# Kernel optimization log

Hardware: AMD Instinct MI355X
Metric: run time of the kernel (lower is better)

## Reference

```python
import jax, jax.numpy as jnp
import numpy as np
from jax import lax

D = 2048
B = 8
T = 1024

def setup_inputs() -> dict:
    key = jax.random.key(0)
    ks = jax.random.split(key, 6)
    s = 1.0 / np.sqrt(D)
    return {
        "x": jax.random.normal(ks[0], (B, T, D), dtype=jnp.float32),
        "h0": jnp.zeros((B, D), dtype=jnp.float32),
        "W_in": jax.random.normal(ks[1], (D, D), dtype=jnp.float32) * s,
        "W_x": jax.random.normal(ks[2], (D, D), dtype=jnp.float32) * s,
        "W_h": jax.random.normal(ks[3], (D, D), dtype=jnp.float32) * (0.5 * s),
        "b": jnp.zeros((D,), dtype=jnp.float32),
        "log_alpha": jnp.asarray(np.log(0.5), dtype=jnp.float32),
        "W_out": jax.random.normal(ks[4], (D, D), dtype=jnp.float32) * s,
    }


def reference(x, h0, W_in, W_x, W_h, b, log_alpha, W_out):
    # x: [B,T,D] -> in_proj + silu pre-activation
    u = jax.nn.silu(jnp.einsum('btd,ed->bte', x, W_in))  # [B,T,D]
    alpha = jnp.exp(log_alpha)
    # Precompute input contribution for all steps: [T,B,D]
    wx_all = jnp.einsum('btd,ed->tbe', u, W_x) + b

    def step(h_prev, wx_t):
        pre = h_prev @ W_h.T + wx_t                  # [B,D]
        h_new = h_prev + alpha * jnp.tanh(pre)
        out = h_new * jax.nn.silu(h_new)             # self-gating
        return h_new, out

    _, outs = lax.scan(step, h0, wx_all)             # outs: [T,B,D]
    y = jnp.einsum('tbd,ed->bte', outs, W_out)       # out_proj -> [B,T,D]
    return y
```

## Files before the change

### kernel.cpp

```cpp
#include <hip/hip_runtime.h>

#define DEV static __device__ __forceinline__

typedef _Float16 half8  __attribute__((ext_vector_type(8)));
typedef _Float16 half4v __attribute__((ext_vector_type(4)));
typedef float    floatx4 __attribute__((ext_vector_type(4)));
typedef unsigned int u32;
typedef unsigned long long u64;
typedef u32 u32x4 __attribute__((ext_vector_type(4)));

#define SPLIT_S 1024.0f
#define SPLIT_R (1.0f / 1024.0f)

DEV void gl_lds16(const _Float16* g, _Float16* l) {
  __builtin_amdgcn_global_load_lds(
      (const __attribute__((address_space(1))) u32*)g,
      (__attribute__((address_space(3))) u32*)l, 16, 0, 0);
}

DEV u32x4 llc_load16(u64 addr) {
  u32x4 r;
  asm volatile("global_load_dwordx4 %0, %1, off sc0 sc1"
               : "=v"(r) : "v"(addr));
  return r;
}
DEV void llc_store8(u64 addr, u64 v) {
  asm volatile("global_store_dwordx2 %0, %1, off sc0 sc1"
               :: "v"(addr), "v"(v) : "memory");
}
DEV void llc_store4(u64 addr, int v) {
  asm volatile("global_store_dword %0, %1, off sc0 sc1"
               :: "v"(addr), "v"(v) : "memory");
}

DEV float fast_tanh(float x) {
  const float e = __expf(2.0f * fabsf(x));
  return copysignf(1.0f - 2.0f / (1.0f + e), x);
}

__global__ __launch_bounds__(256) void k_convert(
    const float* __restrict__ wout, const float* __restrict__ h0,
    _Float16* __restrict__ WoutF, char* __restrict__ hpub,
    int* __restrict__ flags)
{
  if (blockIdx.x == 0 && threadIdx.x < 128) flags[threadIdx.x] = 0;
  const int NW4 = (2048 * 2048) / 4;
  for (int i = blockIdx.x * 256 + threadIdx.x; i < NW4; i += gridDim.x * 256) {
    const float4 v = ((const float4*)wout)[i];
    half4v o;
    o[0] = (_Float16)v.x; o[1] = (_Float16)v.y;
    o[2] = (_Float16)v.z; o[3] = (_Float16)v.w;
    ((half4v*)WoutF)[i] = o;
  }
  for (int id = blockIdx.x * 256 + threadIdx.x; id < 2048; id += gridDim.x * 256) {
    const int c = id >> 3, b = id & 7;
    union { _Float16 h[8]; u32x4 v; } hi, lo;
#pragma unroll
    for (int j = 0; j < 8; ++j) {
      const float v = h0[b * 2048 + c * 8 + j];
      const _Float16 h = (_Float16)v;
      hi.h[j] = h;
      lo.h[j] = (_Float16)((v - (float)h) * SPLIT_S);
    }
    *(u32x4*)(hpub + c * 128 + b * 16)         = hi.v;
    *(u32x4*)(hpub + 32768 + c * 128 + b * 16) = lo.v;
  }
}

template <int EPI>
__global__ __launch_bounds__(256) void k_gemm_split(
    const float* __restrict__ A, const float* __restrict__ B,
    float* __restrict__ C, const float* __restrict__ bias,
    int M, int N, int K)
{
  __shared__ _Float16 Ah[4096], Al[4096], Bh[4096], Bl[4096];
  const int tid  = threadIdx.x;
  const int lane = tid & 63, wave = tid >> 6;
  const int wm = wave >> 1, wn = wave & 1;
  const int tm = blockIdx.y * 128, tn = blockIdx.x * 128;
  const int lr = lane & 15, lk = lane >> 4;

  floatx4 acch[4][4] = {};
  floatx4 accl[4][4] = {};

  for (int k0 = 0; k0 < K; k0 += 32) {
    float4 av[4], bv[4];
#pragma unroll
    for (int q = 0; q < 4; ++q) {
      const int c = tid + q * 256;
      const int rr = c >> 3, cc = (c & 7) * 4;
      av[q] = *(const float4*)(A + (size_t)(tm + rr) * K + k0 + cc);
      bv[q] = *(const float4*)(B + (size_t)(tn + rr) * K + k0 + cc);
    }
    __syncthreads();
#pragma unroll
    for (int q = 0; q < 4; ++q) {
      const int c = tid + q * 256;
      const int rr = c >> 3, cc = (c & 7) * 4;
      half4v ah, al, bh, bl;
#pragma unroll
      for (int j = 0; j < 4; ++j) {
        const float xa = av[q][j], xb = bv[q][j];
        const _Float16 ha = (_Float16)xa, hb = (_Float16)xb;
        ah[j] = ha; al[j] = (_Float16)((xa - (float)ha) * SPLIT_S);
        bh[j] = hb; bl[j] = (_Float16)((xb - (float)hb) * SPLIT_S);
      }
      *(half4v*)(Ah + rr * 32 + cc) = ah;
      *(half4v*)(Al + rr * 32 + cc) = al;
      *(half4v*)(Bh + rr * 32 + cc) = bh;
      *(half4v*)(Bl + rr * 32 + cc) = bl;
    }
    __syncthreads();

    half8 fah[4], fal[4], fbh[4], fbl[4];
#pragma unroll
    for (int mi = 0; mi < 4; ++mi) {
      const int off = (wm * 64 + mi * 16 + lr) * 32 + lk * 8;
      fah[mi] = *(const half8*)(Ah + off);
      fal[mi] = *(const half8*)(Al + off);
    }
#pragma unroll
    for (int ni = 0; ni < 4; ++ni) {
      const int off = (wn * 64 + ni * 16 + lr) * 32 + lk * 8;
      fbh[ni] = *(const half8*)(Bh + off);
      fbl[ni] = *(const half8*)(Bl + off);
    }
#pragma unroll
    for (int mi = 0; mi < 4; ++mi)
#pragma unroll
      for (int ni = 0; ni < 4; ++ni) {
        acch[mi][ni] = __builtin_amdgcn_mfma_f32_16x16x32_f16(fah[mi], fbh[ni], acch[mi][ni], 0, 0, 0);
        accl[mi][ni] = __builtin_amdgcn_mfma_f32_16x16x32_f16(
            fah[mi], fbl[ni],
            __builtin_amdgcn_mfma_f32_16x16x32_f16(fal[mi], fbh[ni], accl[mi][ni], 0, 0, 0),
            0, 0, 0);
      }
  }

#pragma unroll
  for (int mi = 0; mi < 4; ++mi)
#pragma unroll
    for (int ni = 0; ni < 4; ++ni) {
      const int gcol = tn + wn * 64 + ni * 16 + lr;
#pragma unroll
      for (int r = 0; r < 4; ++r) {
        const int grow = tm + wm * 64 + mi * 16 + lk * 4 + r;
        const float v = acch[mi][ni][r] + accl[mi][ni][r] * SPLIT_R;
        if (EPI == 0) {
          C[(size_t)grow * N + gcol] = v / (1.0f + __expf(-v));
        } else {
          const int tt = grow & 1023, bb = grow >> 10;
          C[(size_t)(tt * 8 + bb) * N + gcol] = v + bias[gcol];
        }
      }
    }
}

__global__ __launch_bounds__(256) void k_gemm_out(
    const _Float16* __restrict__ A, const _Float16* __restrict__ B,
    float* __restrict__ C, int M, int N, int K)
{
  __shared__ _Float16 As[4096];
  __shared__ _Float16 Bs[4096];
  const int tid  = threadIdx.x;
  const int lane = tid & 63, wave = tid >> 6;
  const int wm = wave >> 1, wn = wave & 1;
  const int tm = blockIdx.y * 128, tn = blockIdx.x * 128;
  const int lr = lane & 15, lk = lane >> 4;
  const int r0 = tid >> 2;
  const int c0 = (tid & 3) * 8;

  floatx4 acc[4][4] = {};

  for (int k0 = 0; k0 < K; k0 += 32) {
#pragma unroll
    for (int c = 0; c < 2; ++c) {
      const int row = c * 64 + r0;
      gl_lds16(A + (size_t)(tm + row) * K + k0 + c0, As + c * 2048 + wave * 512);
      gl_lds16(B + (size_t)(tn + row) * K + k0 + c0, Bs + c * 2048 + wave * 512);
    }
    __syncthreads();

    half8 af[4], bf[4];
#pragma unroll
    for (int mi = 0; mi < 4; ++mi)
      af[mi] = *(const half8*)(As + (wm * 64 + mi * 16 + lr) * 32 + lk * 8);
#pragma unroll
    for (int ni = 0; ni < 4; ++ni)
      bf[ni] = *(const half8*)(Bs + (wn * 64 + ni * 16 + lr) * 32 + lk * 8);
#pragma unroll
    for (int mi = 0; mi < 4; ++mi)
#pragma unroll
      for (int ni = 0; ni < 4; ++ni)
        acc[mi][ni] = __builtin_amdgcn_mfma_f32_16x16x32_f16(af[mi], bf[ni], acc[mi][ni], 0, 0, 0);
    __syncthreads();
  }

#pragma unroll
  for (int mi = 0; mi < 4; ++mi)
#pragma unroll
    for (int ni = 0; ni < 4; ++ni) {
      const int gcol = tn + wn * 64 + ni * 16 + lr;
#pragma unroll
      for (int r = 0; r < 4; ++r) {
        const int grow = tm + wm * 64 + mi * 16 + lk * 4 + r;
        C[(size_t)grow * N + gcol] = acc[mi][ni][r] * 8.0f;
      }
    }
}

__global__ __launch_bounds__(256, 1) void k_recur(
    const float* __restrict__ Wh, const float* __restrict__ wxp,
    const float* __restrict__ h0p, const float* __restrict__ lalpha,
    _Float16* __restrict__ outs, char* __restrict__ h_pub, int* flags)
{
  __shared__ float red[256 * 4];
  const int tid = threadIdx.x;
  const int lane = tid & 63, wave = tid >> 6;
  const int g = blockIdx.x;
  const int e0 = g * 16;
  const int lr = lane & 15, lk = lane >> 4;
  const int lrc = lr & 7;
  const float alpha = __expf(lalpha[0]);

  half8 afh[16], afl[16];
#pragma unroll
  for (int ks = 0; ks < 16; ++ks) {
    const float* wp = Wh + (size_t)(e0 + lr) * 2048 + wave * 512 + ks * 32 + lk * 8;
    const float4 f0 = *(const float4*)wp;
    const float4 f1 = *(const float4*)(wp + 4);
    half8 h, l;
#pragma unroll
    for (int j = 0; j < 4; ++j) {
      const float a0 = ((const float*)&f0)[j], a1 = ((const float*)&f1)[j];
      const _Float16 h0_ = (_Float16)a0;
      const _Float16 h1_ = (_Float16)a1;
      h[j]     = h0_; l[j]     = (_Float16)((a0 - (float)h0_) * SPLIT_S);
      h[j + 4] = h1_; l[j + 4] = (_Float16)((a1 - (float)h1_) * SPLIT_S);
    }
    afh[ks] = h; afl[ks] = l;
  }

  const bool owner = (tid < 64) && (lr < 8);
  float hr0 = 0.f, hr1 = 0.f, hr2 = 0.f, hr3 = 0.f;
  if (owner) {
    const float4 hv = *(const float4*)(h0p + (size_t)lr * 2048 + e0 + lk * 4);
    hr0 = hv.x; hr1 = hv.y; hr2 = hv.z; hr3 = hv.w;
  }

  const u64 hbase = (u64)h_pub;
  const u64 flag_base = (u64)flags;
  const u64 gb_off = (u64)((wave * 64 + lk) * 128 + lrc * 16);

  for (int t = 0; t < 1024; ++t) {
    float4 wv = {0.f, 0.f, 0.f, 0.f};
    if (owner) wv = *(const float4*)(wxp + (size_t)(t * 8 + lr) * 2048 + e0 + lk * 4);

    if (t > 0 && wave == 0) {
      const u64* fp = (const u64*)flags + lane;
      for (;;) {
        const u64 fv = __hip_atomic_load(fp, __ATOMIC_RELAXED, __HIP_MEMORY_SCOPE_AGENT);
        if (__all(((int)fv >= t) && ((int)(fv >> 32) >= t))) break;
        __builtin_amdgcn_s_sleep(1);
      }
    }
    __syncthreads();

    const u64 pb = hbase + (u64)(t & 1) * 65536 + gb_off;
    u32x4 sh[16], sl[16];
#pragma unroll
    for (int ks = 0; ks < 16; ++ks) sh[ks] = llc_load16(pb + (u64)ks * 512);
#pragma unroll
    for (int ks = 0; ks < 16; ++ks) sl[ks] = llc_load16(pb + 32768 + (u64)ks * 512);
    asm volatile("s_waitcnt vmcnt(16)" ::: "memory");
    __builtin_amdgcn_sched_barrier(0);

    floatx4 ph[4] = {};
    floatx4 pl[4] = {};
#pragma unroll
    for (int ks = 0; ks < 16; ++ks) {
      const half8 bh = __builtin_bit_cast(half8, sh[ks]);
      ph[ks & 3] = __builtin_amdgcn_mfma_f32_16x16x32_f16(afh[ks], bh, ph[ks & 3], 0, 0, 0);
      pl[ks & 3] = __builtin_amdgcn_mfma_f32_16x16x32_f16(afl[ks], bh, pl[ks & 3], 0, 0, 0);
    }
    asm volatile("s_waitcnt vmcnt(0)" ::: "memory");
    __builtin_amdgcn_sched_barrier(0);

#pragma unroll
    for (int ks = 0; ks < 16; ++ks) {
      const half8 bl = __builtin_bit_cast(half8, sl[ks]);
      pl[ks & 3] = __builtin_amdgcn_mfma_f32_16x16x32_f16(afh[ks], bl, pl[ks & 3], 0, 0, 0);
    }
    const floatx4 pt = (ph[0] + ph[1] + ph[2] + ph[3]) +
                       (pl[0] + pl[1] + pl[2] + pl[3]) * SPLIT_R;
    *(floatx4*)&red[(wave * 64 + lane) * 4] = pt;
    __syncthreads();

    if (tid < 64) {
      const floatx4* R = (const floatx4*)red;
      const floatx4 s = R[lane] + R[64 + lane] + R[128 + lane] + R[192 + lane];
      union { _Float16 h[4]; u64 u; } hv, lv, ov;
      if (owner) {
        hr0 += alpha * fast_tanh(s[0] + wv.x);
        hr1 += alpha * fast_tanh(s[1] + wv.y);
        hr2 += alpha * fast_tanh(s[2] + wv.z);
        hr3 += alpha * fast_tanh(s[3] + wv.w);
        hv.h[0] = (_Float16)hr0; hv.h[1] = (_Float16)hr1;
        hv.h[2] = (_Float16)hr2; hv.h[3] = (_Float16)hr3;
        lv.h[0] = (_Float16)((hr0 - (float)hv.h[0]) * SPLIT_S);
        lv.h[1] = (_Float16)((hr1 - (float)hv.h[1]) * SPLIT_S);
        lv.h[2] = (_Float16)((hr2 - (float)hv.h[2]) * SPLIT_S);
        lv.h[3] = (_Float16)((hr3 - (float)hv.h[3]) * SPLIT_S);
        const u64 dst = hbase + (u64)((t + 1) & 1) * 65536 +
                        (u64)((2 * g + (lk >> 1)) * 128 + lr * 16 + (lk & 1) * 8);
        llc_store8(dst,         hv.u);
        llc_store8(dst + 32768, lv.u);
      }
      asm volatile("s_waitcnt vmcnt(0)" ::: "memory");
      if (lane == 0) llc_store4(flag_base + (u64)g * 4, t + 1);
      if (owner) {
        ov.h[0] = (_Float16)((hr0 * hr0 / (1.f + __expf(-hr0))) * 0.125f);
        ov.h[1] = (_Float16)((hr1 * hr1 / (1.f + __expf(-hr1))) * 0.125f);
        ov.h[2] = (_Float16)((hr2 * hr2 / (1.f + __expf(-hr2))) * 0.125f);
        ov.h[3] = (_Float16)((hr3 * hr3 / (1.f + __expf(-hr3))) * 0.125f);
        *(u64*)(outs + (size_t)(lr * 1024 + t) * 2048 + e0 + lk * 4) = ov.u;
      }
    }
  }
}

extern "C" void kernel_launch(void* const* d_in, const int* in_sizes, int n_in,
                              void* d_out, int out_size, void* d_ws, size_t ws_size,
                              hipStream_t stream)
{
  (void)in_sizes; (void)n_in; (void)out_size; (void)ws_size;
  const float* x    = (const float*)d_in[0];
  const float* h0   = (const float*)d_in[1];
  const float* Win  = (const float*)d_in[2];
  const float* Wx   = (const float*)d_in[3];
  const float* Wh   = (const float*)d_in[4];
  const float* bias = (const float*)d_in[5];
  const float* lal  = (const float*)d_in[6];
  const float* Wout = (const float*)d_in[7];

  char* ws = (char*)d_ws;
  float*    U     = (float*)(ws);
  _Float16* OUTS  = (_Float16*)(ws);
  _Float16* WoutF = (_Float16*)(ws + 67108864);
  char*     hpub  = ws + 75497472;
  int*      flags = (int*)(ws + 75628544);
  float*    wxbuf = (float*)d_out;

  const dim3 gg(16, 64);

  k_convert<<<512, 256, 0, stream>>>(Wout, h0, WoutF, hpub, flags);
  k_gemm_split<0><<<gg, 256, 0, stream>>>(x, Win, U, nullptr, 8192, 2048, 2048);
  k_gemm_split<1><<<gg, 256, 0, stream>>>(U, Wx, wxbuf, bias, 8192, 2048, 2048);
  k_recur<<<128, 256, 0, stream>>>(Wh, wxbuf, h0, lal, OUTS, hpub, flags);
  k_gemm_out<<<gg, 256, 0, stream>>>(OUTS, WoutF, (float*)d_out, 8192, 2048, 2048);
}
```

Measured before the change: 4.513 ms.

## Halve recurrence blocks to 64 with 32 columns each; publish via atomic swaps

The persistent recurrence kernel now runs on 64 blocks, each owning 32 hidden columns, so there are two 16-row MFMA tiles per wave and every lane of wave 0 owns outputs. This halves the number of flags each block polls per step and the number of cross-block participants in the per-step barrier. Hidden-state and flag publication switch from sc0/sc1 stores to global atomic swaps, which are meant to resolve at the shared cache level. The cost is twice the MFMA work and register-held weights per block, with fewer CUs active.

```diff
diff --git a/kernel.cpp b/kernel.cpp
--- a/kernel.cpp
+++ b/kernel.cpp
@@ -24,12 +24,12 @@
                : "=v"(r) : "v"(addr));
   return r;
 }
-DEV void llc_store8(u64 addr, u64 v) {
-  asm volatile("global_store_dwordx2 %0, %1, off sc0 sc1"
+DEV void mall_swap8(u64 addr, u64 v) {
+  asm volatile("global_atomic_swap_x2 %0, %1, off"
                :: "v"(addr), "v"(v) : "memory");
 }
-DEV void llc_store4(u64 addr, int v) {
-  asm volatile("global_store_dword %0, %1, off sc0 sc1"
+DEV void mall_swap4(u64 addr, int v) {
+  asm volatile("global_atomic_swap %0, %1, off"
                :: "v"(addr), "v"(v) : "memory");
 }
 
@@ -43,7 +43,7 @@
     _Float16* __restrict__ WoutF, char* __restrict__ hpub,
     int* __restrict__ flags)
 {
-  if (blockIdx.x == 0 && threadIdx.x < 128) flags[threadIdx.x] = 0;
+  if (blockIdx.x == 0 && threadIdx.x < 64) flags[threadIdx.x] = 0;
   const int NW4 = (2048 * 2048) / 4;
   for (int i = blockIdx.x * 256 + threadIdx.x; i < NW4; i += gridDim.x * 256) {
     const float4 v = ((const float4*)wout)[i];
@@ -214,37 +214,40 @@
     const float* __restrict__ h0p, const float* __restrict__ lalpha,
     _Float16* __restrict__ outs, char* __restrict__ h_pub, int* flags)
 {
-  __shared__ float red[256 * 4];
+  __shared__ float red[8 * 64 * 4];
   const int tid = threadIdx.x;
   const int lane = tid & 63, wave = tid >> 6;
   const int g = blockIdx.x;
-  const int e0 = g * 16;
+  const int e0 = g * 32;
   const int lr = lane & 15, lk = lane >> 4;
   const int lrc = lr & 7;
   const float alpha = __expf(lalpha[0]);
 
-  half8 afh[16], afl[16];
-#pragma unroll
-  for (int ks = 0; ks < 16; ++ks) {
-    const float* wp = Wh + (size_t)(e0 + lr) * 2048 + wave * 512 + ks * 32 + lk * 8;
-    const float4 f0 = *(const float4*)wp;
-    const float4 f1 = *(const float4*)(wp + 4);
-    half8 h, l;
-#pragma unroll
-    for (int j = 0; j < 4; ++j) {
-      const float a0 = ((const float*)&f0)[j], a1 = ((const float*)&f1)[j];
-      const _Float16 h0_ = (_Float16)a0;
-      const _Float16 h1_ = (_Float16)a1;
-      h[j]     = h0_; l[j]     = (_Float16)((a0 - (float)h0_) * SPLIT_S);
-      h[j + 4] = h1_; l[j + 4] = (_Float16)((a1 - (float)h1_) * SPLIT_S);
-    }
-    afh[ks] = h; afl[ks] = l;
-  }
-
-  const bool owner = (tid < 64) && (lr < 8);
+  half8 afh[2][16], afl[2][16];
+#pragma unroll
+  for (int m = 0; m < 2; ++m)
+#pragma unroll
+    for (int ks = 0; ks < 16; ++ks) {
+      const float* wp = Wh + (size_t)(e0 + m * 16 + lr) * 2048 + wave * 512 + ks * 32 + lk * 8;
+      const float4 f0 = *(const float4*)wp;
+      const float4 f1 = *(const float4*)(wp + 4);
+      half8 h, l;
+#pragma unroll
+      for (int j = 0; j < 4; ++j) {
+        const float a0 = ((const float*)&f0)[j], a1 = ((const float*)&f1)[j];
+        const _Float16 h0_ = (_Float16)a0;
+        const _Float16 h1_ = (_Float16)a1;
+        h[j]     = h0_; l[j]     = (_Float16)((a0 - (float)h0_) * SPLIT_S);
+        h[j + 4] = h1_; l[j + 4] = (_Float16)((a1 - (float)h1_) * SPLIT_S);
+      }
+      afh[m][ks] = h; afl[m][ks] = l;
+    }
+
+  const int ob = lane & 7, ocg = lane >> 3;
+  const bool owner = (tid < 64);
   float hr0 = 0.f, hr1 = 0.f, hr2 = 0.f, hr3 = 0.f;
   if (owner) {
-    const float4 hv = *(const float4*)(h0p + (size_t)lr * 2048 + e0 + lk * 4);
+    const float4 hv = *(const float4*)(h0p + (size_t)ob * 2048 + e0 + ocg * 4);
     hr0 = hv.x; hr1 = hv.y; hr2 = hv.z; hr3 = hv.w;
   }
 
@@ -254,13 +257,14 @@
 
   for (int t = 0; t < 1024; ++t) {
     float4 wv = {0.f, 0.f, 0.f, 0.f};
-    if (owner) wv = *(const float4*)(wxp + (size_t)(t * 8 + lr) * 2048 + e0 + lk * 4);
+    if (owner) wv = *(const float4*)(wxp + (size_t)(t * 8 + ob) * 2048 + e0 + ocg * 4);
 
     if (t > 0 && wave == 0) {
-      const u64* fp = (const u64*)flags + lane;
+      const u64* fp = (const u64*)flags + (lane & 31);
       for (;;) {
         const u64 fv = __hip_atomic_load(fp, __ATOMIC_RELAXED, __HIP_MEMORY_SCOPE_AGENT);
-        if (__all(((int)fv >= t) && ((int)(fv >> 32) >= t))) break;
+        const bool ok = (lane < 32) ? (((int)fv >= t) && ((int)(fv >> 32) >= t)) : true;
+        if (__all(ok)) break;
         __builtin_amdgcn_s_sleep(1);
       }
     }
@@ -275,13 +279,15 @@
     asm volatile("s_waitcnt vmcnt(16)" ::: "memory");
     __builtin_amdgcn_sched_barrier(0);
 
-    floatx4 ph[4] = {};
-    floatx4 pl[4] = {};
+    floatx4 ph[2][2] = {};
+    floatx4 pl[2][2] = {};
 #pragma unroll
     for (int ks = 0; ks < 16; ++ks) {
       const half8 bh = __builtin_bit_cast(half8, sh[ks]);
-      ph[ks & 3] = __builtin_amdgcn_mfma_f32_16x16x32_f16(afh[ks], bh, ph[ks & 3], 0, 0, 0);
-      pl[ks & 3] = __builtin_amdgcn_mfma_f32_16x16x32_f16(afl[ks], bh, pl[ks & 3], 0, 0, 0);
+      ph[0][ks & 1] = __builtin_amdgcn_mfma_f32_16x16x32_f16(afh[0][ks], bh, ph[0][ks & 1], 0, 0, 0);
+      pl[0][ks & 1] = __builtin_amdgcn_mfma_f32_16x16x32_f16(afl[0][ks], bh, pl[0][ks & 1], 0, 0, 0);
+      ph[1][ks & 1] = __builtin_amdgcn_mfma_f32_16x16x32_f16(afh[1][ks], bh, ph[1][ks & 1], 0, 0, 0);
+      pl[1][ks & 1] = __builtin_amdgcn_mfma_f32_16x16x32_f16(afl[1][ks], bh, pl[1][ks & 1], 0, 0, 0);
     }
     asm volatile("s_waitcnt vmcnt(0)" ::: "memory");
     __builtin_amdgcn_sched_barrier(0);
@@ -289,42 +295,45 @@
 #pragma unroll
     for (int ks = 0; ks < 16; ++ks) {
       const half8 bl = __builtin_bit_cast(half8, sl[ks]);
-      pl[ks & 3] = __builtin_amdgcn_mfma_f32_16x16x32_f16(afh[ks], bl, pl[ks & 3], 0, 0, 0);
-    }
-    const floatx4 pt = (ph[0] + ph[1] + ph[2] + ph[3]) +
-                       (pl[0] + pl[1] + pl[2] + pl[3]) * SPLIT_R;
-    *(floatx4*)&red[(wave * 64 + lane) * 4] = pt;
-    __syncthreads();
-
-    if (tid < 64) {
+      pl[0][ks & 1] = __builtin_amdgcn_mfma_f32_16x16x32_f16(afh[0][ks], bl, pl[0][ks & 1], 0, 0, 0);
+      pl[1][ks & 1] = __builtin_amdgcn_mfma_f32_16x16x32_f16(afh[1][ks], bl, pl[1][ks & 1], 0, 0, 0);
+    }
+#pragma unroll
+    for (int m = 0; m < 2; ++m) {
+      const floatx4 pt = (ph[m][0] + ph[m][1]) + (pl[m][0] + pl[m][1]) * SPLIT_R;
+      *(floatx4*)&red[((wave * 2 + m) * 64 + lane) * 4] = pt;
+    }
+    __syncthreads();
+
+    if (owner) {
       const floatx4* R = (const floatx4*)red;
-      const floatx4 s = R[lane] + R[64 + lane] + R[128 + lane] + R[192 + lane];
+      const int fi = (ocg & 3) * 16 + ob;
+      const int mm = ocg >> 2;
+      const floatx4 s = R[(0 * 2 + mm) * 64 + fi] + R[(1 * 2 + mm) * 64 + fi] +
+                        R[(2 * 2 + mm) * 64 + fi] + R[(3 * 2 + mm) * 64 + fi];
       union { _Float16 h[4]; u64 u; } hv, lv, ov;
-      if (owner) {
-        hr0 += alpha * fast_tanh(s[0] + wv.x);
-        hr1 += alpha * fast_tanh(s[1] + wv.y);
-        hr2 += alpha * fast_tanh(s[2] + wv.z);
-        hr3 += alpha * fast_tanh(s[3] + wv.w);
-        hv.h[0] = (_Float16)hr0; hv.h[1] = (_Float16)hr1;
-        hv.h[2] = (_Float16)hr2; hv.h[3] = (_Float16)hr3;
-        lv.h[0] = (_Float16)((hr0 - (float)hv.h[0]) * SPLIT_S);
-        lv.h[1] = (_Float16)((hr1 - (float)hv.h[1]) * SPLIT_S);
-        lv.h[2] = (_Float16)((hr2 - (float)hv.h[2]) * SPLIT_S);
-        lv.h[3] = (_Float16)((hr3 - (float)hv.h[3]) * SPLIT_S);
-        const u64 dst = hbase + (u64)((t + 1) & 1) * 65536 +
-                        (u64)((2 * g + (lk >> 1)) * 128 + lr * 16 + (lk & 1) * 8);
-        llc_store8(dst,         hv.u);
-        llc_store8(dst + 32768, lv.u);
-      }
+      hr0 += alpha * fast_tanh(s[0] + wv.x);
+      hr1 += alpha * fast_tanh(s[1] + wv.y);
+      hr2 += alpha * fast_tanh(s[2] + wv.z);
+      hr3 += alpha * fast_tanh(s[3] + wv.w);
+      hv.h[0] = (_Float16)hr0; hv.h[1] = (_Float16)hr1;
+      hv.h[2] = (_Float16)hr2; hv.h[3] = (_Float16)hr3;
+      lv.h[0] = (_Float16)((hr0 - (float)hv.h[0]) * SPLIT_S);
+      lv.h[1] = (_Float16)((hr1 - (float)hv.h[1]) * SPLIT_S);
+      lv.h[2] = (_Float16)((hr2 - (float)hv.h[2]) * SPLIT_S);
+      lv.h[3] = (_Float16)((hr3 - (float)hv.h[3]) * SPLIT_S);
+      const u64 dst = hbase + (u64)((t + 1) & 1) * 65536 +
+                      (u64)((4 * g + (ocg >> 1)) * 128 + ob * 16 + (ocg & 1) * 8);
+      mall_swap8(dst,         hv.u);
+      mall_swap8(dst + 32768, lv.u);
       asm volatile("s_waitcnt vmcnt(0)" ::: "memory");
-      if (lane == 0) llc_store4(flag_base + (u64)g * 4, t + 1);
-      if (owner) {
-        ov.h[0] = (_Float16)((hr0 * hr0 / (1.f + __expf(-hr0))) * 0.125f);
-        ov.h[1] = (_Float16)((hr1 * hr1 / (1.f + __expf(-hr1))) * 0.125f);
-        ov.h[2] = (_Float16)((hr2 * hr2 / (1.f + __expf(-hr2))) * 0.125f);
-        ov.h[3] = (_Float16)((hr3 * hr3 / (1.f + __expf(-hr3))) * 0.125f);
-        *(u64*)(outs + (size_t)(lr * 1024 + t) * 2048 + e0 + lk * 4) = ov.u;
-      }
+      if (lane == 0) mall_swap4(flag_base + (u64)g * 4, t + 1);
+      ov.h[0] = (_Float16)((hr0 * hr0 / (1.f + __expf(-hr0))) * 0.125f);
+      ov.h[1] = (_Float16)((hr1 * hr1 / (1.f + __expf(-hr1))) * 0.125f);
+      ov.h[2] = (_Float16)((hr2 * hr2 / (1.f + __expf(-hr2))) * 0.125f);
+      ov.h[3] = (_Float16)((hr3 * hr3 / (1.f + __expf(-hr3))) * 0.125f);
+      *(u64*)(outs + (size_t)(ob * 1024 + t) * 2048 + e0 + ocg * 4) = ov.u;
+    } else if (tid == 64) {
     }
   }
 }
@@ -356,6 +365,6 @@
   k_convert<<<512, 256, 0, stream>>>(Wout, h0, WoutF, hpub, flags);
   k_gemm_split<0><<<gg, 256, 0, stream>>>(x, Win, U, nullptr, 8192, 2048, 2048);
   k_gemm_split<1><<<gg, 256, 0, stream>>>(U, Wx, wxbuf, bias, 8192, 2048, 2048);
-  k_recur<<<128, 256, 0, stream>>>(Wh, wxbuf, h0, lal, OUTS, hpub, flags);
+  k_recur<<<64, 256, 0, stream>>>(Wh, wxbuf, h0, lal, OUTS, hpub, flags);
   k_gemm_out<<<gg, 256, 0, stream>>>(OUTS, WoutF, (float*)d_out, 8192, 2048, 2048);
 }
```

New measurement: 4.653 ms. +3.1%, slower.

## Pre-split U and W_x into fp16 hi/lo pairs for second GEMM

Applied to the files above, without the earlier changes.

The first GEMM epilogue now writes the SiLU output as fp16 hi/lo halves instead of fp32, and W_x is pre-split into hi/lo fp16 by the convert kernel. The second GEMM then streams these halves directly into LDS with global_load_lds, skipping the per-tile fp32-to-split conversion in registers. W_out conversion moves to a separate kernel after gemm2 so it can reuse U's workspace region. This trades an extra kernel launch and an extra W_x conversion pass for lighter loads and less ALU work in the second GEMM.

```diff
diff --git a/kernel.cpp b/kernel.cpp
--- a/kernel.cpp
+++ b/kernel.cpp
@@ -39,11 +39,43 @@
 }
 
 __global__ __launch_bounds__(256) void k_convert(
-    const float* __restrict__ wout, const float* __restrict__ h0,
-    _Float16* __restrict__ WoutF, char* __restrict__ hpub,
-    int* __restrict__ flags)
+    const float* __restrict__ wx, const float* __restrict__ h0,
+    _Float16* __restrict__ Wxhi, _Float16* __restrict__ Wxlo,
+    char* __restrict__ hpub, int* __restrict__ flags)
 {
   if (blockIdx.x == 0 && threadIdx.x < 128) flags[threadIdx.x] = 0;
+  const int NW4 = (2048 * 2048) / 4;
+  for (int i = blockIdx.x * 256 + threadIdx.x; i < NW4; i += gridDim.x * 256) {
+    const float4 v = ((const float4*)wx)[i];
+    half4v h, l;
+#pragma unroll
+    for (int j = 0; j < 4; ++j) {
+      const float a = ((const float*)&v)[j];
+      const _Float16 hh = (_Float16)a;
+      h[j] = hh;
+      l[j] = (_Float16)((a - (float)hh) * SPLIT_S);
+    }
+    ((half4v*)Wxhi)[i] = h;
+    ((half4v*)Wxlo)[i] = l;
+  }
+  for (int id = blockIdx.x * 256 + threadIdx.x; id < 2048; id += gridDim.x * 256) {
+    const int c = id >> 3, b = id & 7;
+    union { _Float16 h[8]; u32x4 v; } hi, lo;
+#pragma unroll
+    for (int j = 0; j < 8; ++j) {
+      const float v = h0[b * 2048 + c * 8 + j];
+      const _Float16 h = (_Float16)v;
+      hi.h[j] = h;
+      lo.h[j] = (_Float16)((v - (float)h) * SPLIT_S);
+    }
+    *(u32x4*)(hpub + c * 128 + b * 16)         = hi.v;
+    *(u32x4*)(hpub + 32768 + c * 128 + b * 16) = lo.v;
+  }
+}
+
+__global__ __launch_bounds__(256) void k_convert2(
+    const float* __restrict__ wout, _Float16* __restrict__ WoutF)
+{
   const int NW4 = (2048 * 2048) / 4;
   for (int i = blockIdx.x * 256 + threadIdx.x; i < NW4; i += gridDim.x * 256) {
     const float4 v = ((const float4*)wout)[i];
@@ -52,25 +84,11 @@
     o[2] = (_Float16)v.z; o[3] = (_Float16)v.w;
     ((half4v*)WoutF)[i] = o;
   }
-  for (int id = blockIdx.x * 256 + threadIdx.x; id < 2048; id += gridDim.x * 256) {
-    const int c = id >> 3, b = id & 7;
-    union { _Float16 h[8]; u32x4 v; } hi, lo;
-#pragma unroll
-    for (int j = 0; j < 8; ++j) {
-      const float v = h0[b * 2048 + c * 8 + j];
-      const _Float16 h = (_Float16)v;
-      hi.h[j] = h;
-      lo.h[j] = (_Float16)((v - (float)h) * SPLIT_S);
-    }
-    *(u32x4*)(hpub + c * 128 + b * 16)         = hi.v;
-    *(u32x4*)(hpub + 32768 + c * 128 + b * 16) = lo.v;
-  }
-}
-
-template <int EPI>
-__global__ __launch_bounds__(256) void k_gemm_split(
+}
+
+__global__ __launch_bounds__(256) void k_gemm1(
     const float* __restrict__ A, const float* __restrict__ B,
-    float* __restrict__ C, const float* __restrict__ bias,
+    _Float16* __restrict__ Chi, _Float16* __restrict__ Clo,
     int M, int N, int K)
 {
   __shared__ _Float16 Ah[4096], Al[4096], Bh[4096], Bl[4096];
@@ -146,12 +164,82 @@
       for (int r = 0; r < 4; ++r) {
         const int grow = tm + wm * 64 + mi * 16 + lk * 4 + r;
         const float v = acch[mi][ni][r] + accl[mi][ni][r] * SPLIT_R;
-        if (EPI == 0) {
-          C[(size_t)grow * N + gcol] = v / (1.0f + __expf(-v));
-        } else {
-          const int tt = grow & 1023, bb = grow >> 10;
-          C[(size_t)(tt * 8 + bb) * N + gcol] = v + bias[gcol];
-        }
+        const float s = v / (1.0f + __expf(-v));
+        const _Float16 sh = (_Float16)s;
+        Chi[(size_t)grow * N + gcol] = sh;
+        Clo[(size_t)grow * N + gcol] = (_Float16)((s - (float)sh) * SPLIT_S);
+      }
+    }
+}
+
+__global__ __launch_bounds__(256) void k_gemm2(
+    const _Float16* __restrict__ Ahi, const _Float16* __restrict__ Alo,
+    const _Float16* __restrict__ Bhi, const _Float16* __restrict__ Blo,
+    float* __restrict__ C, const float* __restrict__ bias,
+    int M, int N, int K)
+{
+  __shared__ _Float16 Ah[4096], Al[4096], Bh[4096], Bl[4096];
+  const int tid  = threadIdx.x;
+  const int lane = tid & 63, wave = tid >> 6;
+  const int wm = wave >> 1, wn = wave & 1;
+  const int tm = blockIdx.y * 128, tn = blockIdx.x * 128;
+  const int lr = lane & 15, lk = lane >> 4;
+  const int r0 = tid >> 2;
+  const int c0 = (tid & 3) * 8;
+
+  floatx4 acch[4][4] = {};
+  floatx4 accl[4][4] = {};
+
+  for (int k0 = 0; k0 < K; k0 += 32) {
+#pragma unroll
+    for (int c = 0; c < 2; ++c) {
+      const int row = c * 64 + r0;
+      const size_t aoff = (size_t)(tm + row) * K + k0 + c0;
+      const size_t boff = (size_t)(tn + row) * K + k0 + c0;
+      gl_lds16(Ahi + aoff, Ah + c * 2048 + wave * 512);
+      gl_lds16(Alo + aoff, Al + c * 2048 + wave * 512);
+      gl_lds16(Bhi + boff, Bh + c * 2048 + wave * 512);
+      gl_lds16(Blo + boff, Bl + c * 2048 + wave * 512);
+    }
+    __syncthreads();
+
+    half8 fah[4], fal[4], fbh[4], fbl[4];
+#pragma unroll
+    for (int mi = 0; mi < 4; ++mi) {
+      const int off = (wm * 64 + mi * 16 + lr) * 32 + lk * 8;
+      fah[mi] = *(const half8*)(Ah + off);
+      fal[mi] = *(const half8*)(Al + off);
+    }
+#pragma unroll
+    for (int ni = 0; ni < 4; ++ni) {
+      const int off = (wn * 64 + ni * 16 + lr) * 32 + lk * 8;
+      fbh[ni] = *(const half8*)(Bh + off);
+      fbl[ni] = *(const half8*)(Bl + off);
+    }
+#pragma unroll
+    for (int mi = 0; mi < 4; ++mi)
+#pragma unroll
+      for (int ni = 0; ni < 4; ++ni) {
+        acch[mi][ni] = __builtin_amdgcn_mfma_f32_16x16x32_f16(fah[mi], fbh[ni], acch[mi][ni], 0, 0, 0);
+        accl[mi][ni] = __builtin_amdgcn_mfma_f32_16x16x32_f16(
+            fah[mi], fbl[ni],
+            __builtin_amdgcn_mfma_f32_16x16x32_f16(fal[mi], fbh[ni], accl[mi][ni], 0, 0, 0),
+            0, 0, 0);
+      }
+    __syncthreads();
+  }
+
+#pragma unroll
+  for (int mi = 0; mi < 4; ++mi)
+#pragma unroll
+    for (int ni = 0; ni < 4; ++ni) {
+      const int gcol = tn + wn * 64 + ni * 16 + lr;
+#pragma unroll
+      for (int r = 0; r < 4; ++r) {
+        const int grow = tm + wm * 64 + mi * 16 + lk * 4 + r;
+        const float v = acch[mi][ni][r] + accl[mi][ni][r] * SPLIT_R;
+        const int tt = grow & 1023, bb = grow >> 10;
+        C[(size_t)(tt * 8 + bb) * N + gcol] = v + bias[gcol];
       }
     }
 }
@@ -344,18 +432,22 @@
   const float* Wout = (const float*)d_in[7];
 
   char* ws = (char*)d_ws;
-  float*    U     = (float*)(ws);
+  _Float16* Uhi   = (_Float16*)(ws);
+  _Float16* Ulo   = (_Float16*)(ws + 33554432);
   _Float16* OUTS  = (_Float16*)(ws);
-  _Float16* WoutF = (_Float16*)(ws + 67108864);
-  char*     hpub  = ws + 75497472;
-  int*      flags = (int*)(ws + 75628544);
+  _Float16* WoutF = (_Float16*)(ws + 33554432);
+  _Float16* Wxhi  = (_Float16*)(ws + 67108864);
+  _Float16* Wxlo  = (_Float16*)(ws + 75497472);
+  char*     hpub  = ws + 83886080;
+  int*      flags = (int*)(ws + 84017152);
   float*    wxbuf = (float*)d_out;
 
   const dim3 gg(16, 64);
 
-  k_convert<<<512, 256, 0, stream>>>(Wout, h0, WoutF, hpub, flags);
-  k_gemm_split<0><<<gg, 256, 0, stream>>>(x, Win, U, nullptr, 8192, 2048, 2048);
-  k_gemm_split<1><<<gg, 256, 0, stream>>>(U, Wx, wxbuf, bias, 8192, 2048, 2048);
+  k_convert<<<512, 256, 0, stream>>>(Wx, h0, Wxhi, Wxlo, hpub, flags);
+  k_gemm1<<<gg, 256, 0, stream>>>(x, Win, Uhi, Ulo, 8192, 2048, 2048);
+  k_gemm2<<<gg, 256, 0, stream>>>(Uhi, Ulo, Wxhi, Wxlo, wxbuf, bias, 8192, 2048, 2048);
+  k_convert2<<<512, 256, 0, stream>>>(Wout, WoutF);
   k_recur<<<128, 256, 0, stream>>>(Wh, wxbuf, h0, lal, OUTS, hpub, flags);
   k_gemm_out<<<gg, 256, 0, stream>>>(OUTS, WoutF, (float*)d_out, 8192, 2048, 2048);
 }
```

Result: no change. 4.464 ms (-1.1%).
